# Performance work log

Measured on AMD Instinct MI355X. Metric: run time of the kernel, lower is better.

The kernel has to match this reference:

```python
import jax, jax.numpy as jnp
import numpy as np

HID, PROJ, ATTN = 512, 1024, 128
B, L = 4, 2048


def _apply_rope(x):
    # x: [B, L, 2, ATTN]; RoPE over sequence dim (axis=1)
    half = x.shape[-1] // 2
    inv_freq = jnp.power(10000.0, -jnp.arange(half, dtype=jnp.float32) / half)
    pos = jnp.arange(x.shape[1], dtype=x.dtype)
    sinusoid = pos[:, None] * inv_freq.astype(x.dtype)          # [L, half]
    sin = jnp.sin(sinusoid)[None, :, None, :]                   # [1, L, 1, half]
    cos = jnp.cos(sinusoid)[None, :, None, :]
    x1, x2 = jnp.split(x, 2, axis=-1)
    return jnp.concatenate([x1 * cos - x2 * sin, x2 * cos + x1 * sin], axis=-1)


def setup_inputs() -> dict:
    key = jax.random.key(0)
    ks = jax.random.split(key, 8)
    node = jax.random.normal(ks[0], (B, L, HID), dtype=jnp.float32)
    bias = jax.random.normal(ks[1], (B, L, L), dtype=jnp.float32)
    scaling = jnp.full((1,), ATTN ** -0.5, dtype=jnp.float32)
    w1 = jax.random.normal(ks[2], (HID, 2 * PROJ + ATTN), dtype=jnp.float32) * (HID ** -0.5)
    b1 = jnp.zeros((2 * PROJ + ATTN,), dtype=jnp.float32)
    ms_weight = jax.random.normal(ks[3], (2, ATTN), dtype=jnp.float32) * 0.02
    ms_bias = jnp.zeros((2, ATTN), dtype=jnp.float32)
    w2 = jax.random.normal(ks[4], (PROJ, HID), dtype=jnp.float32) * (PROJ ** -0.5)
    b2 = jnp.zeros((HID,), dtype=jnp.float32)
    return {"node": node, "bias": bias, "scaling": scaling, "w1": w1, "b1": b1,
            "ms_weight": ms_weight, "ms_bias": ms_bias, "w2": w2, "b2": b2}


def reference(node, bias, scaling, w1, b1, ms_weight, ms_bias, w2, b2):
    # gated projection + SiLU
    gva = jax.nn.silu(node @ w1 + b1)                           # [B, L, 2P+A]
    gates, values, base = jnp.split(gva, [PROJ, 2 * PROJ], axis=-1)
    # multi-headed scaling -> [B, L, 2, A], then RoPE, then split q/k
    qk = base[..., None, :] * ms_weight + ms_bias               # [B, L, 2, A]
    qk = _apply_rope(qk)
    q, k = qk[..., 0, :], qk[..., 1, :]                         # [B, L, A]
    logits = jnp.einsum('bid,bjd->bij', q * scaling, k) + bias  # [B, L, L]
    attn = jax.nn.softmax(logits, axis=-1)
    out = jnp.einsum('bij,bjd->bid', attn, values)              # [B, L, P]
    return (out * gates) @ w2 + b2                              # [B, L, HID]
```

## Files before the change

kernel.cpp:

```cpp
#include <hip/hip_runtime.h>
#include <math.h>

#define HIDN 512
#define PROJ 1024
#define ATTN 128
#define BATCH 4
#define SEQ 2048
#define N1 (2*PROJ+ATTN)
#define ROWS (BATCH*SEQ)

typedef __attribute__((ext_vector_type(4))) float f32x4;
typedef __attribute__((ext_vector_type(8))) short bf16x8;

__device__ __forceinline__ short f2bf(float x){
    unsigned u = __builtin_bit_cast(unsigned, x);
    unsigned rounding = 0x7fffu + ((u >> 16) & 1u);
    u += rounding;
    return (short)(u >> 16);
}
__device__ __forceinline__ float bf2f(short s){
    unsigned u = ((unsigned)(unsigned short)s) << 16;
    return __builtin_bit_cast(float, u);
}

__device__ __forceinline__ void gload16(const void* g, void* l){
    __builtin_amdgcn_global_load_lds((const __attribute__((address_space(1))) void*)g,
                                     (__attribute__((address_space(3))) void*)l,
                                     16, 0, 0);
}

template<int BK, class Epi>
__device__ __forceinline__ void gemm_bt_tile(const short* __restrict__ A, int lda,
                                             const short* __restrict__ BT, int ldb,
                                             int m0, int n0, int K, Epi epi)
{
    __shared__ __align__(16) short lA[2][128*BK];
    __shared__ __align__(16) short lB[2][128*BK];
    const int t = threadIdx.x;
    const int lane = t & 63;
    const int w = t >> 6;
    const int wr = (w >> 1) * 64, wc = (w & 1) * 64;
    const int half = lane >> 4, l16 = lane & 15;
    constexpr int SPT = BK/16;

    f32x4 acc[4][4];
    #pragma unroll
    for (int i=0;i<4;i++)
        #pragma unroll
        for (int j=0;j<4;j++)
            acc[i][j] = (f32x4){0.f,0.f,0.f,0.f};

    auto stage = [&](int buf, int k0){
        #pragma unroll
        for (int i = 0; i < SPT; i++) {
            int li = i*256 + t;
            int r = li / (BK/8), s = li % (BK/8);
            int ss = (BK==64) ? (s ^ (r & 7)) : (s ^ ((r >> 1) & 3));
            gload16(A + (size_t)(m0+r)*lda + k0 + ss*8, lA[buf] + li*8);
        }
        #pragma unroll
        for (int i = 0; i < SPT; i++) {
            int li = i*256 + t;
            int r = li / (BK/8), s = li % (BK/8);
            int ss = (BK==64) ? (s ^ (r & 7)) : (s ^ ((r >> 1) & 3));
            gload16(BT + (size_t)(n0+r)*ldb + k0 + ss*8, lB[buf] + li*8);
        }
    };

    stage(0, 0);
    __syncthreads();
    int cur = 0;
    for (int k0 = BK; k0 <= K; k0 += BK) {
        if (k0 < K) stage(cur^1, k0);
        #pragma unroll
        for (int kk = 0; kk < BK; kk += 32) {
            bf16x8 af[4], bfr[4];
            const int cs = (kk >> 3) + half;
            #pragma unroll
            for (int i=0;i<4;i++){
                int row = wr + i*16 + l16;
                int sl = (BK==64) ? (cs ^ (row & 7)) : (cs ^ ((row >> 1) & 3));
                af[i] = *(const bf16x8*)(lA[cur] + row*BK + sl*8);
            }
            #pragma unroll
            for (int j=0;j<4;j++){
                int row = wc + j*16 + l16;
                int sl = (BK==64) ? (cs ^ (row & 7)) : (cs ^ ((row >> 1) & 3));
                bfr[j] = *(const bf16x8*)(lB[cur] + row*BK + sl*8);
            }
            #pragma unroll
            for (int i=0;i<4;i++)
                #pragma unroll
                for (int j=0;j<4;j++)
                    acc[i][j] = __builtin_amdgcn_mfma_f32_16x16x32_bf16(af[i], bfr[j], acc[i][j], 0, 0, 0);
        }
        __syncthreads();
        cur ^= 1;
    }
    #pragma unroll
    for (int i=0;i<4;i++)
        #pragma unroll
        for (int j=0;j<4;j++)
            #pragma unroll
            for (int q=0;q<4;q++)
                epi(m0 + wr + i*16 + half*4 + q, n0 + wc + j*16 + l16, acc[i][j][q]);
}

__global__ void k_cast_node(const float* __restrict__ in, short* __restrict__ out){
    int idx = blockIdx.x*256 + threadIdx.x;
    const float4 v = ((const float4*)in)[idx];
    short4 o; o.x = f2bf(v.x); o.y = f2bf(v.y); o.z = f2bf(v.z); o.w = f2bf(v.w);
    ((short4*)out)[idx] = o;
}

__global__ void k_transpose_cast(const float* __restrict__ in, short* __restrict__ out,
                                 int R, int C){
    __shared__ short tile[64][65];
    int r0 = blockIdx.y*64, c0 = blockIdx.x*64;
    int t = threadIdx.x;
    #pragma unroll
    for (int i=0;i<16;i++){
        int lin = i*256 + t; int r = lin>>6, c = lin&63;
        tile[r][c] = f2bf(in[(size_t)(r0+r)*C + c0+c]);
    }
    __syncthreads();
    #pragma unroll
    for (int i=0;i<16;i++){
        int lin = i*256 + t; int c = lin>>6, r = lin&63;
        out[(size_t)(c0+c)*R + r0+r] = tile[r][c];
    }
}

__global__ void k_transpose_v(const short* __restrict__ values, short* __restrict__ VT){
    __shared__ short tile[64][65];
    int z = blockIdx.z;
    int c0 = blockIdx.x*64, r0 = blockIdx.y*64;
    int t = threadIdx.x;
    #pragma unroll
    for (int i=0;i<16;i++){
        int lin = i*256 + t; int r = lin>>6, c = lin&63;
        tile[r][c] = values[(size_t)(z*SEQ + r0+r)*PROJ + c0+c];
    }
    __syncthreads();
    #pragma unroll
    for (int i=0;i<16;i++){
        int lin = i*256 + t; int c = lin>>6, r = lin&63;
        VT[((size_t)z*PROJ + c0+c)*SEQ + r0+r] = tile[r][c];
    }
}

__global__ __launch_bounds__(256) void k_mm1(const short* __restrict__ nodeb,
        const short* __restrict__ w1T, const float* __restrict__ b1,
        short* __restrict__ gates, short* __restrict__ values, short* __restrict__ baseb){
    int b = blockIdx.x;
    int wg = (b & 7) * (N1/128*64/8) + (b >> 3);
    int n0 = (wg % (N1/128))*128, m0 = (wg / (N1/128))*128;
    gemm_bt_tile<32>(nodeb, HIDN, w1T, HIDN, m0, n0, HIDN,
        [=](int row, int col, float v){
            v += b1[col];
            v = v / (1.f + __expf(-v));
            short bv = f2bf(v);
            if (col < PROJ)        gates [(size_t)row*PROJ + col]        = bv;
            else if (col < 2*PROJ) values[(size_t)row*PROJ + col-PROJ]   = bv;
            else                   baseb [(size_t)row*ATTN + col-2*PROJ] = bv;
        });
}

__global__ void k_rope2(const short* __restrict__ baseb, const float* __restrict__ msw,
                        const float* __restrict__ msb, const float* __restrict__ scaling,
                        short* __restrict__ qb, short* __restrict__ kb){
    int idx = blockIdx.x*256 + threadIdx.x;
    int d = idx & 63;
    int row = idx >> 6;
    int l = row & (SEQ-1);
    float inv = exp2f(-(float)d * (13.287712379549449f/64.f));
    float ang = (float)l * inv;
    float s = sinf(ang), c = cosf(ang);
    const short* bp = baseb + (size_t)row*ATTN;
    float b_lo = bf2f(bp[d]), b_hi = bf2f(bp[d+64]);
    float x1q = b_lo*msw[d]        + msb[d];
    float x2q = b_hi*msw[d+64]     + msb[d+64];
    float x1k = b_lo*msw[128+d]    + msb[128+d];
    float x2k = b_hi*msw[128+d+64] + msb[128+d+64];
    float sc = scaling[0];
    qb[(size_t)row*ATTN + d]    = f2bf((x1q*c - x2q*s)*sc);
    qb[(size_t)row*ATTN + d+64] = f2bf((x2q*c + x1q*s)*sc);
    kb[(size_t)row*ATTN + d]    = f2bf(x1k*c - x2k*s);
    kb[(size_t)row*ATTN + d+64] = f2bf(x2k*c + x1k*s);
}

__global__ __launch_bounds__(256) void k_qksm(
        const short* __restrict__ qg, const short* __restrict__ kg,
        const float* __restrict__ bias, short* __restrict__ P,
        float* __restrict__ lsum16)
{
    __shared__ __align__(16) short smem[32768];
    __shared__ float sl[2][128];

    const int b = blockIdx.x;
    const int wg = (b & 7) * 128 + (b >> 3);
    const int z  = wg >> 8;
    const int qt = (wg >> 4) & 15;
    const int kt = wg & 15;
    const int q0 = qt * 128, kv0 = kt * 128;

    const int t = threadIdx.x;
    const int lane = t & 63, w = t >> 6;
    const int wr = (w >> 1)*64, wc = (w & 1)*64;
    const int half = lane >> 4, l16 = lane & 15;

    const short* Kg = kg + ((size_t)z*SEQ + kv0)*ATTN;
    const short* Qg = qg + ((size_t)z*SEQ + q0)*ATTN;

    #pragma unroll
    for (int i = 0; i < 8; i++) {
        int li = i*256 + t;
        int r = li >> 4, s = li & 15;
        int ss = s ^ (r & 15);
        gload16(Kg + (size_t)r*ATTN + ss*8, smem + li*8);
        gload16(Qg + (size_t)r*ATTN + ss*8, smem + 16384 + li*8);
    }

    f32x4 acc[4][4];
    #pragma unroll
    for (int i=0;i<4;i++)
        #pragma unroll
        for (int j=0;j<4;j++)
            acc[i][j] = *(const f32x4*)(bias
                + ((size_t)z*SEQ + q0 + wc + j*16 + l16)*SEQ
                + kv0 + wr + i*16 + half*4);

    __syncthreads();

    #pragma unroll
    for (int kk = 0; kk < 128; kk += 32) {
        const int cs = (kk >> 3) + half;
        bf16x8 af[4], bfr[4];
        #pragma unroll
        for (int i=0;i<4;i++){
            int row = wr + i*16 + l16;
            af[i] = *(const bf16x8*)(smem + row*128 + (cs ^ (row & 15))*8);
        }
        #pragma unroll
        for (int j=0;j<4;j++){
            int row = wc + j*16 + l16;
            bfr[j] = *(const bf16x8*)(smem + 16384 + row*128 + (cs ^ (row & 15))*8);
        }
        #pragma unroll
        for (int i=0;i<4;i++)
            #pragma unroll
            for (int j=0;j<4;j++)
                acc[i][j] = __builtin_amdgcn_mfma_f32_16x16x32_bf16(af[i], bfr[j], acc[i][j], 0, 0, 0);
    }

    __syncthreads();

    short* pt = smem;
    float tsum[4];
    #pragma unroll
    for (int j=0;j<4;j++){
        int col = wc + j*16 + l16;
        float sj = 0.f;
        #pragma unroll
        for (int i=0;i<4;i++){
            float p0=__expf(acc[i][j][0]), p1=__expf(acc[i][j][1]);
            float p2=__expf(acc[i][j][2]), p3=__expf(acc[i][j][3]);
            sj += p0+p1+p2+p3;
            short4 pv; pv.x=f2bf(p0); pv.y=f2bf(p1); pv.z=f2bf(p2); pv.w=f2bf(p3);
            *(short4*)(pt + col*136 + wr + i*16 + half*4) = pv;
        }
        tsum[j] = sj;
    }
    #pragma unroll
    for (int j=0;j<4;j++){
        tsum[j] += __shfl_xor(tsum[j],16,64);
        tsum[j] += __shfl_xor(tsum[j],32,64);
    }
    if (half==0){
        #pragma unroll
        for (int j=0;j<4;j++) sl[wr>>6][wc + j*16 + l16] = tsum[j];
    }
    __syncthreads();

    short* Pp = P + ((size_t)z*SEQ + q0)*SEQ + kv0;
    #pragma unroll
    for (int i=0;i<8;i++){
        int idx = i*256 + t;
        int q = idx >> 4, g = idx & 15;
        *(bf16x8*)(Pp + (size_t)q*SEQ + g*8) = *(const bf16x8*)(pt + q*136 + g*8);
    }
    if (t < 128)
        lsum16[(size_t)kt*ROWS + (size_t)z*SEQ + q0 + t] = sl[0][t] + sl[1][t];
}

__global__ void k_combine(const float* __restrict__ lsum16, float* __restrict__ linv){
    int r = blockIdx.x*256 + threadIdx.x;
    float s = 0.f;
    #pragma unroll
    for (int kt=0; kt<16; kt++) s += lsum16[(size_t)kt*ROWS + r];
    linv[r] = 1.f/s;
}

__global__ __launch_bounds__(256) void k_pv2(const short* __restrict__ P,
        const short* __restrict__ VT, const short* __restrict__ gates,
        const float* __restrict__ linv, short* __restrict__ a2){
    int b = blockIdx.x;
    int wg = (b & 7) * 64 + (b >> 3);
    int xx = wg & 7, yy = (wg >> 3) & 15, z = wg >> 7;
    const short* A = P  + (size_t)z*SEQ*SEQ;
    const short* B = VT + (size_t)z*PROJ*SEQ;
    int n0 = xx*128, m0 = yy*128;
    gemm_bt_tile<64>(A, SEQ, B, SEQ, m0, n0, SEQ,
        [=](int r, int c, float v){
            size_t ri = (size_t)z*SEQ + r;
            size_t gi = ri*PROJ + c;
            a2[gi] = f2bf(v * linv[ri] * bf2f(gates[gi]));
        });
}

__global__ __launch_bounds__(256) void k_mm2(const short* __restrict__ a2,
        const short* __restrict__ w2T, const float* __restrict__ b2,
        float* __restrict__ out){
    int b = blockIdx.x;
    int wg = (b & 7) * 32 + (b >> 3);
    int n0 = (wg & 3)*128, m0 = (wg >> 2)*128;
    gemm_bt_tile<32>(a2, PROJ, w2T, PROJ, m0, n0, PROJ,
        [=](int r, int c, float v){
            out[(size_t)r*HIDN + c] = v + b2[c];
        });
}

extern "C" void kernel_launch(void* const* d_in, const int* in_sizes, int n_in,
                              void* d_out, int out_size, void* d_ws, size_t ws_size,
                              hipStream_t stream) {
    const float* node    = (const float*)d_in[0];
    const float* bias    = (const float*)d_in[1];
    const float* scaling = (const float*)d_in[2];
    const float* w1      = (const float*)d_in[3];
    const float* b1      = (const float*)d_in[4];
    const float* msw     = (const float*)d_in[5];
    const float* msb     = (const float*)d_in[6];
    const float* w2      = (const float*)d_in[7];
    const float* b2      = (const float*)d_in[8];
    float* out = (float*)d_out;

    char* p = (char*)d_ws;
    auto alloc = [&](size_t bytes){ char* r = p; p += (bytes + 255) & ~(size_t)255; return r; };
    short* nodeb  = (short*)alloc((size_t)ROWS*HIDN*2);
    short* w1T    = (short*)alloc((size_t)N1*HIDN*2);
    short* w2T    = (short*)alloc((size_t)HIDN*PROJ*2);
    short* gates  = (short*)alloc((size_t)ROWS*PROJ*2);
    short* values = (short*)alloc((size_t)ROWS*PROJ*2);
    short* VT     = (short*)alloc((size_t)BATCH*PROJ*SEQ*2);
    short* baseb  = (short*)alloc((size_t)ROWS*ATTN*2);
    short* qb     = (short*)alloc((size_t)ROWS*ATTN*2);
    short* kb     = (short*)alloc((size_t)ROWS*ATTN*2);
    short* Pbuf   = (short*)alloc((size_t)BATCH*SEQ*SEQ*2);
    float* lsum16 = (float*)alloc((size_t)16*ROWS*4);
    float* linv   = (float*)alloc((size_t)ROWS*4);
    short* a2buf  = (short*)alloc((size_t)ROWS*PROJ*2);

    k_cast_node<<<ROWS*HIDN/1024, 256, 0, stream>>>(node, nodeb);
    k_transpose_cast<<<dim3(N1/64, HIDN/64), 256, 0, stream>>>(w1, w1T, HIDN, N1);
    k_transpose_cast<<<dim3(HIDN/64, PROJ/64), 256, 0, stream>>>(w2, w2T, PROJ, HIDN);
    k_mm1<<<(N1/128)*(ROWS/128), 256, 0, stream>>>(nodeb, w1T, b1, gates, values, baseb);
    k_transpose_v<<<dim3(PROJ/64, SEQ/64, BATCH), 256, 0, stream>>>(values, VT);
    k_rope2<<<ROWS*64/256, 256, 0, stream>>>(baseb, msw, msb, scaling, qb, kb);
    k_qksm<<<16*16*BATCH, 256, 0, stream>>>(qb, kb, bias, Pbuf, lsum16);
    k_combine<<<ROWS/256, 256, 0, stream>>>(lsum16, linv);
    k_pv2<<<(PROJ/128)*(SEQ/128)*BATCH, 256, 0, stream>>>(Pbuf, VT, gates, linv, a2buf);
    k_mm2<<<(HIDN/128)*(ROWS/128), 256, 0, stream>>>(a2buf, w2T, b2, out);
}
```

Baseline: 152.2 us.

## Split first projection into 256x128-tile gates/values GEMM and separate base GEMM

The first projection GEMM now uses a 256x128 tile with 512 threads (8 waves) for the gates/values columns, choosing the output buffer once per block instead of branching per element. The 128-column base projection moves to its own small kernel using the original 128x128 tile. The larger tile is meant to raise operand reuse and cut epilogue branching, at the cost of more LDS, fewer blocks, and an extra launch.

```diff
diff --git a/kernel.cpp b/kernel.cpp
--- a/kernel.cpp
+++ b/kernel.cpp
@@ -106,6 +106,80 @@
                 epi(m0 + wr + i*16 + half*4 + q, n0 + wc + j*16 + l16, acc[i][j][q]);
 }
 
+template<class Epi>
+__device__ __forceinline__ void gemm_bt_tile256(const short* __restrict__ A, int lda,
+                                                const short* __restrict__ BT, int ldb,
+                                                int m0, int n0, int K, Epi epi)
+{
+    constexpr int BK = 32;
+    __shared__ __align__(16) short lA[2][256*BK];
+    __shared__ __align__(16) short lB[2][128*BK];
+    const int t = threadIdx.x;
+    const int lane = t & 63;
+    const int w = t >> 6;
+    const int wr = (w >> 1) * 64;
+    const int wc = (w & 1) * 64;
+    const int half = lane >> 4, l16 = lane & 15;
+
+    f32x4 acc[4][4];
+    #pragma unroll
+    for (int i=0;i<4;i++)
+        #pragma unroll
+        for (int j=0;j<4;j++)
+            acc[i][j] = (f32x4){0.f,0.f,0.f,0.f};
+
+    auto stage = [&](int buf, int k0){
+        #pragma unroll
+        for (int i = 0; i < 2; i++) {
+            int li = i*512 + t;
+            int r = li >> 2, s = li & 3;
+            int ss = s ^ ((r >> 1) & 3);
+            gload16(A + (size_t)(m0+r)*lda + k0 + ss*8, lA[buf] + li*8);
+        }
+        {
+            int li = t;
+            int r = li >> 2, s = li & 3;
+            int ss = s ^ ((r >> 1) & 3);
+            gload16(BT + (size_t)(n0+r)*ldb + k0 + ss*8, lB[buf] + li*8);
+        }
+    };
+
+    stage(0, 0);
+    __syncthreads();
+    int cur = 0;
+    for (int k0 = BK; k0 <= K; k0 += BK) {
+        if (k0 < K) stage(cur^1, k0);
+        {
+            bf16x8 af[4], bfr[4];
+            const int cs = half;
+            #pragma unroll
+            for (int i=0;i<4;i++){
+                int row = wr + i*16 + l16;
+                af[i] = *(const bf16x8*)(lA[cur] + row*BK + (cs ^ ((row >> 1) & 3))*8);
+            }
+            #pragma unroll
+            for (int j=0;j<4;j++){
+                int row = wc + j*16 + l16;
+                bfr[j] = *(const bf16x8*)(lB[cur] + row*BK + (cs ^ ((row >> 1) & 3))*8);
+            }
+            #pragma unroll
+            for (int i=0;i<4;i++)
+                #pragma unroll
+                for (int j=0;j<4;j++)
+                    acc[i][j] = __builtin_amdgcn_mfma_f32_16x16x32_bf16(af[i], bfr[j], acc[i][j], 0, 0, 0);
+        }
+        __syncthreads();
+        cur ^= 1;
+    }
+    #pragma unroll
+    for (int i=0;i<4;i++)
+        #pragma unroll
+        for (int j=0;j<4;j++)
+            #pragma unroll
+            for (int q=0;q<4;q++)
+                epi(m0 + wr + i*16 + half*4 + q, n0 + wc + j*16 + l16, acc[i][j][q]);
+}
+
 __global__ void k_cast_node(const float* __restrict__ in, short* __restrict__ out){
     int idx = blockIdx.x*256 + threadIdx.x;
     const float4 v = ((const float4*)in)[idx];
@@ -149,20 +223,33 @@
     }
 }
 
-__global__ __launch_bounds__(256) void k_mm1(const short* __restrict__ nodeb,
+__global__ __launch_bounds__(512) void k_mm1(const short* __restrict__ nodeb,
         const short* __restrict__ w1T, const float* __restrict__ b1,
-        short* __restrict__ gates, short* __restrict__ values, short* __restrict__ baseb){
+        short* __restrict__ gates, short* __restrict__ values){
     int b = blockIdx.x;
-    int wg = (b & 7) * (N1/128*64/8) + (b >> 3);
-    int n0 = (wg % (N1/128))*128, m0 = (wg / (N1/128))*128;
-    gemm_bt_tile<32>(nodeb, HIDN, w1T, HIDN, m0, n0, HIDN,
+    int wg = (b & 7) * 64 + (b >> 3);
+    int n0 = (wg & 15) * 128;
+    int m0 = (wg >> 4) * 256;
+    short* dst = (n0 < PROJ) ? gates : values;
+    const int coff = (n0 < PROJ) ? 0 : PROJ;
+    gemm_bt_tile256(nodeb, HIDN, w1T, HIDN, m0, n0, HIDN,
         [=](int row, int col, float v){
             v += b1[col];
             v = v / (1.f + __expf(-v));
-            short bv = f2bf(v);
-            if (col < PROJ)        gates [(size_t)row*PROJ + col]        = bv;
-            else if (col < 2*PROJ) values[(size_t)row*PROJ + col-PROJ]   = bv;
-            else                   baseb [(size_t)row*ATTN + col-2*PROJ] = bv;
+            dst[(size_t)row*PROJ + (col - coff)] = f2bf(v);
+        });
+}
+
+__global__ __launch_bounds__(256) void k_mmbase(const short* __restrict__ nodeb,
+        const short* __restrict__ w1T, const float* __restrict__ b1,
+        short* __restrict__ baseb){
+    int m0 = blockIdx.x * 128;
+    const short* BT = w1T + (size_t)(2*PROJ)*HIDN;
+    gemm_bt_tile<32>(nodeb, HIDN, BT, HIDN, m0, 0, HIDN,
+        [=](int row, int col, float v){
+            v += b1[2*PROJ + col];
+            v = v / (1.f + __expf(-v));
+            baseb[(size_t)row*ATTN + col] = f2bf(v);
         });
 }
 
@@ -363,7 +450,8 @@
     k_cast_node<<<ROWS*HIDN/1024, 256, 0, stream>>>(node, nodeb);
     k_transpose_cast<<<dim3(N1/64, HIDN/64), 256, 0, stream>>>(w1, w1T, HIDN, N1);
     k_transpose_cast<<<dim3(HIDN/64, PROJ/64), 256, 0, stream>>>(w2, w2T, PROJ, HIDN);
-    k_mm1<<<(N1/128)*(ROWS/128), 256, 0, stream>>>(nodeb, w1T, b1, gates, values, baseb);
+    k_mm1<<<16*(ROWS/256), 512, 0, stream>>>(nodeb, w1T, b1, gates, values);
+    k_mmbase<<<ROWS/128, 256, 0, stream>>>(nodeb, w1T, b1, baseb);
     k_transpose_v<<<dim3(PROJ/64, SEQ/64, BATCH), 256, 0, stream>>>(values, VT);
     k_rope2<<<ROWS*64/256, 256, 0, stream>>>(baseb, msw, msb, scaling, qb, kb);
     k_qksm<<<16*16*BATCH, 256, 0, stream>>>(qb, kb, bias, Pbuf, lsum16);
```

Result: faster. 148.5 us (-2.4%).
